# Performance work log

Measured on AMD Instinct MI355X. Metric: run time of the kernel, lower is better.

The kernel has to match this reference:

```python
import jax, jax.numpy as jnp
import numpy as np

NUM_HEADS = 8
NUM_GROUPS = 32
EPS = 1e-5

def group_norm(x, w, b):
    # x: [B, C, L]
    B, C, L = x.shape
    xg = x.reshape(B, NUM_GROUPS, C // NUM_GROUPS, L)
    mean = xg.mean(axis=(2, 3), keepdims=True)
    var = xg.var(axis=(2, 3), keepdims=True)
    xg = (xg - mean) * jax.lax.rsqrt(var + EPS)
    return xg.reshape(B, C, L) * w[None, :, None] + b[None, :, None]

def setup_inputs() -> dict:
    key = jax.random.key(0)
    ks = jax.random.split(key, 5)
    B, C, H, W = 16, 512, 32, 32
    x = jax.random.normal(ks[0], (B, C, H, W), dtype=jnp.float32)
    norm_w = jnp.ones((C,), dtype=jnp.float32)
    norm_b = jnp.zeros((C,), dtype=jnp.float32)
    w_qkv = jax.random.normal(ks[1], (3 * C, C), dtype=jnp.float32) * (1.0 / np.sqrt(C))
    b_qkv = jax.random.normal(ks[2], (3 * C,), dtype=jnp.float32) * 0.02
    w_proj = jax.random.normal(ks[3], (C, C), dtype=jnp.float32) * (1.0 / np.sqrt(C))
    b_proj = jax.random.normal(ks[4], (C,), dtype=jnp.float32) * 0.02
    return {"x": x, "norm_w": norm_w, "norm_b": norm_b, "w_qkv": w_qkv,
            "b_qkv": b_qkv, "w_proj": w_proj, "b_proj": b_proj}

def reference(x, norm_w, norm_b, w_qkv, b_qkv, w_proj, b_proj):
    B, C = x.shape[0], x.shape[1]
    L = int(np.prod(x.shape[2:]))
    xf = x.reshape(B, C, L)
    h = group_norm(xf, norm_w, norm_b)
    # 1x1 conv == channel matmul: [3C, C] x [B, C, L] -> [B, 3C, L]
    qkv = jnp.einsum('oc,bcl->bol', w_qkv, h) + b_qkv[None, :, None]
    ch = C // NUM_HEADS
    qkv = qkv.reshape(B * NUM_HEADS, 3 * ch, L)
    q, k, v = qkv[:, :ch], qkv[:, ch:2 * ch], qkv[:, 2 * ch:]
    scale = 1.0 / np.sqrt(np.sqrt(ch))
    weight = jnp.einsum('bct,bcs->bts', q * scale, k * scale)  # [B*H, L, L]
    weight = jax.nn.softmax(weight.astype(jnp.float32), axis=-1).astype(weight.dtype)
    a = jnp.einsum('bts,bcs->bct', weight, v)  # [B*H, ch, L]
    a = a.reshape(B, C, L)
    out = jnp.einsum('oc,bcl->bol', w_proj, a) + b_proj[None, :, None]
    return out  # [B, C, L]
```

## Files before the change

kernel.cpp:

```cpp
#include <hip/hip_runtime.h>
#include <math.h>


typedef _Float16 f16x8 __attribute__((ext_vector_type(8)));
typedef _Float16 f16x4 __attribute__((ext_vector_type(4)));
typedef float f32x4 __attribute__((ext_vector_type(4)));

#define MFMA_K16(A, B, C) __builtin_amdgcn_mfma_f32_16x16x16f16(A, B, C, 0, 0, 0)

__device__ __forceinline__ void async_cp16(const void* g, void* l) {
  __builtin_amdgcn_global_load_lds(
      (const __attribute__((address_space(1))) void*)g,
      (__attribute__((address_space(3))) void*)l, 16, 0, 0);
}

__global__ __launch_bounds__(256) void f32_to_f16(
    const float* __restrict__ src, _Float16* __restrict__ dst, int n4) {
  int i = blockIdx.x * 256 + threadIdx.x;
  if (i < n4) {
    float4 v = ((const float4*)src)[i];
    f16x4 o = {(_Float16)v.x, (_Float16)v.y, (_Float16)v.z, (_Float16)v.w};
    *(f16x4*)&dst[(size_t)i * 4] = o;
  }
}

__global__ __launch_bounds__(256) void gn_kernel(
    const float* __restrict__ x, const float* __restrict__ gw,
    const float* __restrict__ gb, _Float16* __restrict__ hT) {
  const int b = blockIdx.x >> 5;
  const int g = blockIdx.x & 31;
  const size_t base = ((size_t)(b * 512 + g * 16)) * 1024;
  const float4* xp = (const float4*)(x + base);
  const int tid = threadIdx.x;

  float4 vals[16];
  float s = 0.f, sq = 0.f;
#pragma unroll
  for (int r = 0; r < 16; ++r) {
    float4 v = xp[tid + 256 * r];
    vals[r] = v;
    s += v.x + v.y + v.z + v.w;
    sq += v.x * v.x + v.y * v.y + v.z * v.z + v.w * v.w;
  }
  __shared__ float rs[256];
  __shared__ float rq[256];
  rs[tid] = s;
  rq[tid] = sq;
  __syncthreads();
  for (int off = 128; off > 0; off >>= 1) {
    if (tid < off) {
      rs[tid] += rs[tid + off];
      rq[tid] += rq[tid + off];
    }
    __syncthreads();
  }
  const float mean = rs[0] * (1.f / 16384.f);
  const float var = rq[0] * (1.f / 16384.f) - mean * mean;
  const float rinv = rsqrtf(var + 1e-5f);
#pragma unroll
  for (int r = 0; r < 16; ++r) {
    const int c = g * 16 + r;
    const float wc = gw[c] * rinv;
    const float bc = gb[c] - mean * wc;
    vals[r].x = vals[r].x * wc + bc;
    vals[r].y = vals[r].y * wc + bc;
    vals[r].z = vals[r].z * wc + bc;
    vals[r].w = vals[r].w * wc + bc;
  }
  _Float16* hb = hT + ((size_t)b * 1024 + tid * 4) * 512 + g * 16;
#pragma unroll
  for (int li = 0; li < 4; ++li) {
    f16x8 o0, o1;
#pragma unroll
    for (int r = 0; r < 8; ++r) {
      float v0 = li == 0 ? vals[r].x : li == 1 ? vals[r].y
                 : li == 2 ? vals[r].z : vals[r].w;
      float v1 = li == 0 ? vals[8 + r].x : li == 1 ? vals[8 + r].y
                 : li == 2 ? vals[8 + r].z : vals[8 + r].w;
      o0[r] = (_Float16)v0;
      o1[r] = (_Float16)v1;
    }
    *(f16x8*)(hb + (size_t)li * 512) = o0;
    *(f16x8*)(hb + (size_t)li * 512 + 8) = o1;
  }
}

template <typename OutT, bool BIAS_ON_M>
__global__ __launch_bounds__(256) void gemm_tn(
    const _Float16* __restrict__ A, const _Float16* __restrict__ B,
    const float* __restrict__ bias, OutT* __restrict__ Out,
    int M, int N, int K, long sA, long sB) {
  __shared__ __align__(16) char smem[34816];
  _Float16* As = (_Float16*)smem;
  _Float16* Bs = As + 128 * 32;
  const int tid = threadIdx.x;
  const int w = tid >> 6, lane = tid & 63;
  const int lx = lane & 15, quad = lane >> 4;
  const int wm = w >> 1, wn = w & 1;
  const int bn = blockIdx.x * 128, bm = blockIdx.y * 128;
  const int z = blockIdx.z;

  const int cr = w * 16;
  const int lrow = lane >> 2;
  const int lk = (lane & 3) * 8;
  const _Float16* Ag = A + (size_t)z * sA + (size_t)(bm + cr + lrow) * K + lk;
  const _Float16* Bg = B + (size_t)z * sB + (size_t)(bn + cr + lrow) * K + lk;
  _Float16* As0 = &As[cr * 32];
  _Float16* As1 = &As[(cr + 64) * 32];
  _Float16* Bs0 = &Bs[cr * 32];
  _Float16* Bs1 = &Bs[(cr + 64) * 32];

  f32x4 acc[4][4];
#pragma unroll
  for (int i = 0; i < 4; ++i)
#pragma unroll
    for (int j = 0; j < 4; ++j) acc[i][j] = (f32x4){0.f, 0.f, 0.f, 0.f};

  for (int k0 = 0; k0 < K; k0 += 32) {
    __syncthreads();
    async_cp16(Ag + k0, As0);
    async_cp16(Ag + (size_t)64 * K + k0, As1);
    async_cp16(Bg + k0, Bs0);
    async_cp16(Bg + (size_t)64 * K + k0, Bs1);
    __syncthreads();
    f16x8 af[4], bf[4];
#pragma unroll
    for (int mt = 0; mt < 4; ++mt)
      af[mt] = *(const f16x8*)&As[(wm * 64 + mt * 16 + lx) * 32 + quad * 8];
#pragma unroll
    for (int nt = 0; nt < 4; ++nt)
      bf[nt] = *(const f16x8*)&Bs[(wn * 64 + nt * 16 + lx) * 32 + quad * 8];
#pragma unroll
    for (int mt = 0; mt < 4; ++mt)
#pragma unroll
      for (int nt = 0; nt < 4; ++nt)
        acc[mt][nt] = __builtin_amdgcn_mfma_f32_16x16x32_f16(
            af[mt], bf[nt], acc[mt][nt], 0, 0, 0);
  }

  OutT* Ob = Out + (size_t)z * M * N;
  if constexpr (sizeof(OutT) == 2) {
    _Float16* T = (_Float16*)smem;
    __syncthreads();
#pragma unroll
    for (int mt = 0; mt < 4; ++mt) {
      const int m0 = bm + wm * 64 + mt * 16 + quad * 4;
      float bm4[4];
#pragma unroll
      for (int i = 0; i < 4; ++i) bm4[i] = BIAS_ON_M ? bias[m0 + i] : 0.f;
#pragma unroll
      for (int nt = 0; nt < 4; ++nt) {
        const int nl = wn * 64 + nt * 16 + lx;
        const float bn1 = BIAS_ON_M ? 0.f : bias[bn + nl];
        f16x4 o = {(_Float16)(acc[mt][nt][0] + (BIAS_ON_M ? bm4[0] : bn1)),
                   (_Float16)(acc[mt][nt][1] + (BIAS_ON_M ? bm4[1] : bn1)),
                   (_Float16)(acc[mt][nt][2] + (BIAS_ON_M ? bm4[2] : bn1)),
                   (_Float16)(acc[mt][nt][3] + (BIAS_ON_M ? bm4[3] : bn1))};
        *(f16x4*)&T[nl * 136 + wm * 64 + mt * 16 + quad * 4] = o;
      }
    }
    __syncthreads();
#pragma unroll
    for (int j = 0; j < 8; ++j) {
      const int r = j * 16 + (tid >> 4), slot = tid & 15;
      f16x8 vv = *(const f16x8*)&T[r * 136 + slot * 8];
      *(f16x8*)((_Float16*)Ob + (size_t)(bn + r) * M + bm + slot * 8) = vv;
    }
  } else {
    float* T32 = (float*)smem;
#pragma unroll
    for (int p = 0; p < 2; ++p) {
      __syncthreads();
      if (wn == p) {
#pragma unroll
        for (int mt = 0; mt < 4; ++mt) {
          const int m0 = bm + wm * 64 + mt * 16 + quad * 4;
          float bm4[4];
#pragma unroll
          for (int i = 0; i < 4; ++i) bm4[i] = BIAS_ON_M ? bias[m0 + i] : 0.f;
#pragma unroll
          for (int nt = 0; nt < 4; ++nt) {
            const int nl = nt * 16 + lx;
            const float bn1 = BIAS_ON_M ? 0.f : bias[bn + p * 64 + nl];
            float4 o = {acc[mt][nt][0] + (BIAS_ON_M ? bm4[0] : bn1),
                        acc[mt][nt][1] + (BIAS_ON_M ? bm4[1] : bn1),
                        acc[mt][nt][2] + (BIAS_ON_M ? bm4[2] : bn1),
                        acc[mt][nt][3] + (BIAS_ON_M ? bm4[3] : bn1)};
            *(float4*)&T32[nl * 136 + wm * 64 + mt * 16 + quad * 4] = o;
          }
        }
      }
      __syncthreads();
#pragma unroll
      for (int j = 0; j < 8; ++j) {
        const int r = j * 8 + (tid >> 5), slot = tid & 31;
        float4 vv = *(const float4*)&T32[r * 136 + slot * 4];
        *(float4*)((float*)Ob + (size_t)(bn + p * 64 + r) * M + bm + slot * 4) =
            vv;
      }
    }
  }
}

#define LQ 72
#define LV 70
#define QSCALE 0.18033688011112042f

__global__ __launch_bounds__(256) void attn_mfma(
    const _Float16* __restrict__ qkvT, _Float16* __restrict__ aT) {
  __shared__ __align__(16) _Float16 ks[64 * LQ];
  __shared__ __align__(16) _Float16 vs[64 * LV];

  const int tid = threadIdx.x;
  const int w = tid >> 6, lane = tid & 63;
  const int lx = lane & 15, quad = lane >> 4;
  const int bh = blockIdx.x, b = bh >> 3, h = bh & 7;
  const int t0 = blockIdx.y * 128;
  const _Float16* qb = qkvT + (size_t)b * 1024 * 1536 + h * 192;

  f16x8 qf[2][2];
#pragma unroll
  for (int g = 0; g < 2; ++g) {
    const _Float16* qrow = qb + (size_t)(t0 + w * 32 + g * 16 + lx) * 1536;
    qf[g][0] = *(const f16x8*)(qrow + quad * 8);
    qf[g][1] = *(const f16x8*)(qrow + 32 + quad * 8);
#pragma unroll
    for (int j = 0; j < 8; ++j) {
      qf[g][0][j] = qf[g][0][j] * (_Float16)QSCALE;
      qf[g][1][j] = qf[g][1][j] * (_Float16)QSCALE;
    }
  }

  const int kr = tid >> 2, kc = (tid & 3) * 16;
  const int vs2 = (tid >> 3) * 2, vc8 = (tid & 7) * 8;
  const _Float16* kgp = qb + (size_t)kr * 1536 + 64 + kc;
  const _Float16* vgp = qb + (size_t)vs2 * 1536 + 128 + vc8;

  f16x8 kp0 = *(const f16x8*)kgp;
  f16x8 kp1 = *(const f16x8*)(kgp + 8);
  f16x8 vp0 = *(const f16x8*)vgp;
  f16x8 vp1 = *(const f16x8*)(vgp + 1536);

  float l_r[2] = {0.f, 0.f};
  f32x4 oacc[2][4];
#pragma unroll
  for (int g = 0; g < 2; ++g)
#pragma unroll
    for (int mt = 0; mt < 4; ++mt) oacc[g][mt] = (f32x4){0.f, 0.f, 0.f, 0.f};

  for (int s0 = 0; s0 < 1024; s0 += 64) {
    __syncthreads();
    *(f16x8*)&ks[kr * LQ + kc] = kp0;
    *(f16x8*)&ks[kr * LQ + kc + 8] = kp1;
#pragma unroll
    for (int i = 0; i < 8; ++i) {
      union { _Float16 hh[2]; unsigned u; } p;
      p.hh[0] = vp0[i];
      p.hh[1] = vp1[i];
      *(unsigned*)&vs[(vc8 + i) * LV + vs2] = p.u;
    }
    __syncthreads();

    if (s0 + 64 < 1024) {
      const _Float16* kg2 = kgp + (size_t)(s0 + 64) * 1536;
      const _Float16* vg2 = vgp + (size_t)(s0 + 64) * 1536;
      kp0 = *(const f16x8*)kg2;
      kp1 = *(const f16x8*)(kg2 + 8);
      vp0 = *(const f16x8*)vg2;
      vp1 = *(const f16x8*)(vg2 + 1536);
    }

    f32x4 sf[2][4];
#pragma unroll
    for (int sb = 0; sb < 4; ++sb) {
      f16x8 k0 = *(const f16x8*)&ks[(sb * 16 + lx) * LQ + quad * 8];
      f16x8 k1 = *(const f16x8*)&ks[(sb * 16 + lx) * LQ + 32 + quad * 8];
#pragma unroll
      for (int g = 0; g < 2; ++g) {
        f32x4 z = {0.f, 0.f, 0.f, 0.f};
        z = __builtin_amdgcn_mfma_f32_16x16x32_f16(k0, qf[g][0], z, 0, 0, 0);
        sf[g][sb] =
            __builtin_amdgcn_mfma_f32_16x16x32_f16(k1, qf[g][1], z, 0, 0, 0);
      }
    }

    f16x4 pf[2][4];
#pragma unroll
    for (int g = 0; g < 2; ++g) {
      float sum = 0.f;
#pragma unroll
      for (int sb = 0; sb < 4; ++sb) {
        float p0 = __builtin_amdgcn_exp2f(sf[g][sb][0]);
        float p1 = __builtin_amdgcn_exp2f(sf[g][sb][1]);
        float p2 = __builtin_amdgcn_exp2f(sf[g][sb][2]);
        float p3 = __builtin_amdgcn_exp2f(sf[g][sb][3]);
        sum += (p0 + p1) + (p2 + p3);
        pf[g][sb] =
            (f16x4){(_Float16)p0, (_Float16)p1, (_Float16)p2, (_Float16)p3};
      }
      l_r[g] += sum;
    }

#pragma unroll
    for (int kb = 0; kb < 4; ++kb)
#pragma unroll
      for (int mt = 0; mt < 4; ++mt) {
        f16x4 vf = *(const f16x4*)&vs[(mt * 16 + lx) * LV + kb * 16 + quad * 4];
        oacc[0][mt] = MFMA_K16(vf, pf[0][kb], oacc[0][mt]);
        oacc[1][mt] = MFMA_K16(vf, pf[1][kb], oacc[1][mt]);
      }
  }

#pragma unroll
  for (int g = 0; g < 2; ++g) {
    float l = l_r[g];
    l += __shfl_xor(l, 16);
    l += __shfl_xor(l, 32);
    const float linv = 1.f / l;
    _Float16* ob =
        aT + ((size_t)b * 1024 + t0 + w * 32 + g * 16 + lx) * 512 + h * 64;
#pragma unroll
    for (int mt = 0; mt < 4; ++mt) {
      f16x4 o = {(_Float16)(oacc[g][mt][0] * linv),
                 (_Float16)(oacc[g][mt][1] * linv),
                 (_Float16)(oacc[g][mt][2] * linv),
                 (_Float16)(oacc[g][mt][3] * linv)};
      *(f16x4*)&ob[mt * 16 + quad * 4] = o;
    }
  }
}

extern "C" void kernel_launch(void* const* d_in, const int* in_sizes, int n_in,
                              void* d_out, int out_size, void* d_ws,
                              size_t ws_size, hipStream_t stream) {
  const float* x = (const float*)d_in[0];
  const float* norm_w = (const float*)d_in[1];
  const float* norm_b = (const float*)d_in[2];
  const float* w_qkv = (const float*)d_in[3];
  const float* b_qkv = (const float*)d_in[4];
  const float* w_proj = (const float*)d_in[5];
  const float* b_proj = (const float*)d_in[6];
  float* out = (float*)d_out;

  _Float16* hT = (_Float16*)d_ws;
  _Float16* qkvT = hT + (size_t)16 * 1024 * 512;
  _Float16* wq = qkvT + (size_t)16 * 1024 * 1536;
  _Float16* wp = wq + (size_t)1536 * 512;
  _Float16* aT = hT;

  f32_to_f16<<<768, 256, 0, stream>>>(w_qkv, wq, 196608);
  f32_to_f16<<<256, 256, 0, stream>>>(w_proj, wp, 65536);
  gn_kernel<<<512, 256, 0, stream>>>(x, norm_w, norm_b, hT);
  gemm_tn<_Float16, true><<<dim3(8, 12, 16), 256, 0, stream>>>(
      wq, hT, b_qkv, qkvT, 1536, 1024, 512, 0L, 524288L);
  attn_mfma<<<dim3(128, 8), 256, 0, stream>>>(qkvT, aT);
  gemm_tn<float, false><<<dim3(4, 8, 16), 256, 0, stream>>>(
      aT, wp, b_proj, out, 1024, 512, 512, 524288L, 0L);
}
```

Before: 211.9 us.

## Double GEMM K-tile to 64 with XOR-swizzled LDS and merge weight conversions

The GEMM now loads 64-wide K tiles per stage instead of 32, halving the number of barrier pairs per K loop. It applies an XOR swizzle to the LDS column layout to avoid bank conflicts on the wider rows. The two weight-conversion kernels are merged into one launch to save a launch. The LDS footprint grows to 32 KB for A and B, which still fits the existing buffer, but each block does more loading per stage without double buffering.

```diff
diff --git a/kernel.cpp b/kernel.cpp
--- a/kernel.cpp
+++ b/kernel.cpp
@@ -14,13 +14,19 @@
       (__attribute__((address_space(3))) void*)l, 16, 0, 0);
 }
 
-__global__ __launch_bounds__(256) void f32_to_f16(
-    const float* __restrict__ src, _Float16* __restrict__ dst, int n4) {
+__global__ __launch_bounds__(256) void cvt_weights(
+    const float* __restrict__ wq, const float* __restrict__ wp,
+    _Float16* __restrict__ dq, _Float16* __restrict__ dp) {
   int i = blockIdx.x * 256 + threadIdx.x;
-  if (i < n4) {
-    float4 v = ((const float4*)src)[i];
+  if (i < 196608) {
+    float4 v = ((const float4*)wq)[i];
     f16x4 o = {(_Float16)v.x, (_Float16)v.y, (_Float16)v.z, (_Float16)v.w};
-    *(f16x4*)&dst[(size_t)i * 4] = o;
+    *(f16x4*)&dq[(size_t)i * 4] = o;
+  } else {
+    int j = i - 196608;
+    float4 v = ((const float4*)wp)[j];
+    f16x4 o = {(_Float16)v.x, (_Float16)v.y, (_Float16)v.z, (_Float16)v.w};
+    *(f16x4*)&dp[(size_t)j * 4] = o;
   }
 }
 
@@ -92,7 +98,7 @@
     int M, int N, int K, long sA, long sB) {
   __shared__ __align__(16) char smem[34816];
   _Float16* As = (_Float16*)smem;
-  _Float16* Bs = As + 128 * 32;
+  _Float16* Bs = As + 128 * 64;
   const int tid = threadIdx.x;
   const int w = tid >> 6, lane = tid & 63;
   const int lx = lane & 15, quad = lane >> 4;
@@ -100,15 +106,10 @@
   const int bn = blockIdx.x * 128, bm = blockIdx.y * 128;
   const int z = blockIdx.z;
 
-  const int cr = w * 16;
-  const int lrow = lane >> 2;
-  const int lk = (lane & 3) * 8;
-  const _Float16* Ag = A + (size_t)z * sA + (size_t)(bm + cr + lrow) * K + lk;
-  const _Float16* Bg = B + (size_t)z * sB + (size_t)(bn + cr + lrow) * K + lk;
-  _Float16* As0 = &As[cr * 32];
-  _Float16* As1 = &As[(cr + 64) * 32];
-  _Float16* Bs0 = &Bs[cr * 32];
-  _Float16* Bs1 = &Bs[(cr + 64) * 32];
+  const int srow = w * 32 + (lane >> 3);
+  const int scol = (((lane & 7) ^ ((lane >> 3) & 7)) * 8);
+  const _Float16* Ag = A + (size_t)z * sA + (size_t)(bm + srow) * K + scol;
+  const _Float16* Bg = B + (size_t)z * sB + (size_t)(bn + srow) * K + scol;
 
   f32x4 acc[4][4];
 #pragma unroll
@@ -116,32 +117,40 @@
 #pragma unroll
     for (int j = 0; j < 4; ++j) acc[i][j] = (f32x4){0.f, 0.f, 0.f, 0.f};
 
-  for (int k0 = 0; k0 < K; k0 += 32) {
-    __syncthreads();
-    async_cp16(Ag + k0, As0);
-    async_cp16(Ag + (size_t)64 * K + k0, As1);
-    async_cp16(Bg + k0, Bs0);
-    async_cp16(Bg + (size_t)64 * K + k0, Bs1);
-    __syncthreads();
-    f16x8 af[4], bf[4];
-#pragma unroll
-    for (int mt = 0; mt < 4; ++mt)
-      af[mt] = *(const f16x8*)&As[(wm * 64 + mt * 16 + lx) * 32 + quad * 8];
-#pragma unroll
-    for (int nt = 0; nt < 4; ++nt)
-      bf[nt] = *(const f16x8*)&Bs[(wn * 64 + nt * 16 + lx) * 32 + quad * 8];
-#pragma unroll
-    for (int mt = 0; mt < 4; ++mt)
+  const int xa = lx & 7;
+
+  for (int k0 = 0; k0 < K; k0 += 64) {
+    __syncthreads();
+#pragma unroll
+    for (int j = 0; j < 4; ++j) {
+      async_cp16(Ag + (size_t)j * 8 * K + k0, &As[(w * 32 + j * 8) * 64]);
+      async_cp16(Bg + (size_t)j * 8 * K + k0, &Bs[(w * 32 + j * 8) * 64]);
+    }
+    __syncthreads();
+#pragma unroll
+    for (int h = 0; h < 2; ++h) {
+      f16x8 af[4], bf[4];
+#pragma unroll
+      for (int mt = 0; mt < 4; ++mt)
+        af[mt] = *(const f16x8*)&As[(wm * 64 + mt * 16 + lx) * 64 +
+                                    ((h * 4 + quad) ^ xa) * 8];
 #pragma unroll
       for (int nt = 0; nt < 4; ++nt)
-        acc[mt][nt] = __builtin_amdgcn_mfma_f32_16x16x32_f16(
-            af[mt], bf[nt], acc[mt][nt], 0, 0, 0);
-  }
+        bf[nt] = *(const f16x8*)&Bs[(wn * 64 + nt * 16 + lx) * 64 +
+                                    ((h * 4 + quad) ^ xa) * 8];
+#pragma unroll
+      for (int mt = 0; mt < 4; ++mt)
+#pragma unroll
+        for (int nt = 0; nt < 4; ++nt)
+          acc[mt][nt] = __builtin_amdgcn_mfma_f32_16x16x32_f16(
+              af[mt], bf[nt], acc[mt][nt], 0, 0, 0);
+    }
+  }
+  __syncthreads();
 
   OutT* Ob = Out + (size_t)z * M * N;
   if constexpr (sizeof(OutT) == 2) {
     _Float16* T = (_Float16*)smem;
-    __syncthreads();
 #pragma unroll
     for (int mt = 0; mt < 4; ++mt) {
       const int m0 = bm + wm * 64 + mt * 16 + quad * 4;
@@ -348,8 +357,7 @@
   _Float16* wp = wq + (size_t)1536 * 512;
   _Float16* aT = hT;
 
-  f32_to_f16<<<768, 256, 0, stream>>>(w_qkv, wq, 196608);
-  f32_to_f16<<<256, 256, 0, stream>>>(w_proj, wp, 65536);
+  cvt_weights<<<1024, 256, 0, stream>>>(w_qkv, w_proj, wq, wp);
   gn_kernel<<<512, 256, 0, stream>>>(x, norm_w, norm_b, hT);
   gemm_tn<_Float16, true><<<dim3(8, 12, 16), 256, 0, stream>>>(
       wq, hT, b_qkv, qkvT, 1536, 1024, 512, 0L, 524288L);
```

New measurement: 203.1 us. 1.04x faster.
